# Performance work log

Hardware: AMD Instinct MI355X
Metric: run time of the kernel (lower is better)

The kernel has to match this reference:

```python
import jax, jax.numpy as jnp
import numpy as np

NUM_CONTROL_POINTS = 4
# Standard Catmull-Rom spline basis (rows map [1, t, t^2, t^3] monomials to control points)
CATMULL_ROM_BASIS = 0.5 * np.array(
    [[0.0, 2.0, 0.0, 0.0],
     [-1.0, 0.0, 1.0, 0.0],
     [2.0, -5.0, 4.0, -1.0],
     [-1.0, 3.0, -3.0, 1.0]], dtype=np.float32)

BATCH, IN_F, OUT_F = 1024, 512, 512


def setup_inputs() -> dict:
    key = jax.random.key(0)
    k1, k2, k3, k4 = jax.random.split(key, 4)
    inp = jax.random.normal(k1, (BATCH, IN_F), dtype=jnp.float32)
    # phase spans [0, 2*pi) so both spline segments (mask = phase < 1.5*pi) are exercised
    phase = jax.random.uniform(k2, (BATCH,), dtype=jnp.float32) * (2.0 * jnp.pi)
    bound = 1.0 / np.sqrt(IN_F)
    weights = jax.random.uniform(k3, (NUM_CONTROL_POINTS, OUT_F, IN_F), dtype=jnp.float32,
                                 minval=-bound, maxval=bound)
    biases = jax.random.uniform(k4, (NUM_CONTROL_POINTS, OUT_F), dtype=jnp.float32,
                                minval=-bound, maxval=bound)
    return {"input": inp, "phase": phase, "weights": weights, "biases": biases}


def _spline_coeffs(phase):
    # Faithful to the original (including its overwrite bug): tt = [1, t^2, t^3, 0]
    basis = jnp.asarray(CATMULL_ROM_BASIS, dtype=phase.dtype)
    t0 = phase / (1.5 * jnp.pi)
    t1 = (phase - 0.5 * jnp.pi) / (1.5 * jnp.pi)
    ones, zeros = jnp.ones_like(phase), jnp.zeros_like(phase)
    tt0 = jnp.stack([ones, t0 * t0, t0 ** 3, zeros], axis=1)  # (B,4)
    tt1 = jnp.stack([ones, t1 * t1, t1 ** 3, zeros], axis=1)  # (B,4)
    mask = (phase < 1.5 * jnp.pi)[:, None]
    # Selecting per-sample coefficients before the weight contraction is exactly
    # equivalent to where(mask, tt0@B@W, tt1@B@W) since the map is linear in tt.
    return jnp.where(mask, tt0 @ basis, tt1 @ basis)  # (B,4) control-point coeffs


def reference(input, phase, weights, biases):
    c = _spline_coeffs(phase)                       # (B,4)
    # Fused form: apply the 4 shared control-point linear layers, then blend,
    # avoiding the (B,out,in) per-sample weight tensor. Same math as
    # (tt@B@W).reshape(B,out,in) @ input[:,:,None] + b.
    y4 = jnp.einsum('bi,coi->bco', input, weights)  # (B,4,out)
    out = jnp.einsum('bc,bco->bo', c, y4) + c @ biases  # (B,out)
    return out
```

## Files before the change

### kernel.cpp

```cpp
#include <hip/hip_runtime.h>


#define BATCH 1024
#define IN_F  512
#define OUT_F 512

constexpr int BM = 32;
constexpr int BO = 32;
constexpr int BK = 32;
constexpr int KITERS = IN_F / BK;
constexpr int A_ELEMS = BM * BK;
constexpr int TILE_ELEMS = (BM + 4 * BO) * BK;
constexpr int NVEC = TILE_ELEMS / 8;

typedef unsigned short u16;
typedef u16    u16x8  __attribute__((ext_vector_type(8)));
typedef __bf16 bf16x8 __attribute__((ext_vector_type(8)));
typedef float  f32x4  __attribute__((ext_vector_type(4)));

__device__ __forceinline__ u16 f2bits(float f) {
  union { float f; unsigned int u; } v; v.f = f;
  unsigned int u = v.u;
  unsigned int r = u + 0x7fffu + ((u >> 16) & 1u);
  return (u16)(r >> 16);
}

__global__ __launch_bounds__(256)
void PhaseLinear_kernel(const float* __restrict__ inp, const float* __restrict__ ph,
                        const float* __restrict__ wts, const float* __restrict__ bia,
                        float* __restrict__ outp) {
  __shared__ alignas(16) u16 sT[2][TILE_ELEMS];
  __shared__ float sCoef[BM][4];

  const int tid = threadIdx.x;
  const int wv  = tid >> 6;
  const int wo  = wv & 1;
  const int wm  = wv >> 1;
  const int l   = tid & 63;
  const int o0  = blockIdx.x * BO;
  const int b0  = blockIdx.y * BM;

  if (tid < BM) {
    const float PI = 3.14159265358979323846f;
    float p  = ph[b0 + tid];
    float t  = (p < 1.5f * PI) ? (p / (1.5f * PI)) : ((p - 0.5f * PI) / (1.5f * PI));
    float t2 = t * t, t3 = t2 * t;
    sCoef[tid][0] = t3 - 0.5f * t2;
    sCoef[tid][1] = 1.0f - 2.5f * t3;
    sCoef[tid][2] = 0.5f * t2 + 2.0f * t3;
    sCoef[tid][3] = -0.5f * t3;
  }

  const int nv = (tid < NVEC - 512) ? 3 : 2;
  const float* src[3];
  int loff[3];
#pragma unroll
  for (int j = 0; j < 3; ++j) {
    int v = tid + j * 256;
    if (v >= NVEC) { src[j] = inp; loff[j] = 0; continue; }
    int e = v * 8;
    loff[j] = e;
    if (e < A_ELEMS) {
      int row = e >> 5, col = e & 31;
      src[j] = inp + (size_t)(b0 + row) * IN_F + col;
    } else {
      int ep = e - A_ELEMS;
      int r = ep >> 5, col = ep & 31;
      int c = r >> 5, oo = r & 31;
      src[j] = wts + ((size_t)c * OUT_F + o0 + oo) * IN_F + col;
    }
  }

  f32x4 regs[3][2];
#pragma unroll
  for (int j = 0; j < 3; ++j)
    if (j < nv) {
      regs[j][0] = *(const f32x4*)(src[j]);
      regs[j][1] = *(const f32x4*)(src[j] + 4);
    }

  f32x4 acc[4];
#pragma unroll
  for (int c = 0; c < 4; ++c) acc[c] = (f32x4){0.f, 0.f, 0.f, 0.f};

  const int q = l >> 4;
  const int n = l & 15;

  for (int kk = 0; kk < KITERS; ++kk) {
    const int bsel = kk & 1;
    u16* buf = &sT[bsel][0];
#pragma unroll
    for (int j = 0; j < 3; ++j)
      if (j < nv) {
        u16x8 pk;
#pragma unroll
        for (int x = 0; x < 4; ++x) {
          pk[x]     = f2bits(regs[j][0][x]);
          pk[x + 4] = f2bits(regs[j][1][x]);
        }
        *(u16x8*)(buf + loff[j]) = pk;
      }
    if (kk + 1 < KITERS) {
#pragma unroll
      for (int j = 0; j < 3; ++j)
        if (j < nv) {
          regs[j][0] = *(const f32x4*)(src[j] + (kk + 1) * BK);
          regs[j][1] = *(const f32x4*)(src[j] + (kk + 1) * BK + 4);
        }
    }
    __syncthreads();
    const u16* pA = buf;
    const u16* pW = buf + A_ELEMS;
    bf16x8 a0 = *(const bf16x8*)(pA + (wm * 16 + n) * BK + q * 8);
#pragma unroll
    for (int c = 0; c < 4; ++c) {
      bf16x8 wf = *(const bf16x8*)(pW + (c * 32 + wo * 16 + n) * BK + q * 8);
      acc[c] = __builtin_amdgcn_mfma_f32_16x16x32_bf16(a0, wf, acc[c], 0, 0, 0);
    }
  }

  const int o = o0 + wo * 16 + n;
  float bs[4];
#pragma unroll
  for (int c = 0; c < 4; ++c) bs[c] = bia[c * OUT_F + o];

#pragma unroll
  for (int r = 0; r < 4; ++r) {
    const int bl = wm * 16 + q * 4 + r;
    float v = 0.f;
#pragma unroll
    for (int c = 0; c < 4; ++c)
      v += sCoef[bl][c] * (acc[c][r] + bs[c]);
    outp[(size_t)(b0 + bl) * OUT_F + o] = v;
  }
}

extern "C" void kernel_launch(void* const* d_in, const int* in_sizes, int n_in,
                              void* d_out, int out_size, void* d_ws, size_t ws_size,
                              hipStream_t stream) {
  const float* inp = (const float*)d_in[0];
  const float* ph  = (const float*)d_in[1];
  const float* wts = (const float*)d_in[2];
  const float* bia = (const float*)d_in[3];
  float* outp = (float*)d_out;

  dim3 grid(OUT_F / BO, BATCH / BM);
  PhaseLinear_kernel<<<grid, 256, 0, stream>>>(inp, ph, wts, bia, outp);
}
```

Measured before the change: 72.66 us.

## Split K across warps with smaller output tile and shared-memory reduction

Halves the output tile width to 16 and assigns the two pairs of waves to separate halves of the K dimension, so each block does half as many K iterations. The two partial sums are combined through a shared-memory buffer before the spline blend and the store. This doubles the grid size for more parallelism and shortens the serial K loop. The cost is an extra reduction step and barrier, and each input tile is re-read by twice as many blocks.

```diff
diff --git a/kernel.cpp b/kernel.cpp
--- a/kernel.cpp
+++ b/kernel.cpp
@@ -6,11 +6,13 @@
 #define OUT_F 512
 
 constexpr int BM = 32;
-constexpr int BO = 32;
+constexpr int BO = 16;
 constexpr int BK = 32;
-constexpr int KITERS = IN_F / BK;
-constexpr int A_ELEMS = BM * BK;
-constexpr int TILE_ELEMS = (BM + 4 * BO) * BK;
+constexpr int KW = IN_F / 2;
+constexpr int KITERS = KW / BK;
+constexpr int A_ELEMS = 2 * BM * BK;
+constexpr int W_ELEMS = 2 * 4 * BO * BK;
+constexpr int TILE_ELEMS = A_ELEMS + W_ELEMS;
 constexpr int NVEC = TILE_ELEMS / 8;
 
 typedef unsigned short u16;
@@ -31,11 +33,12 @@
                         float* __restrict__ outp) {
   __shared__ alignas(16) u16 sT[2][TILE_ELEMS];
   __shared__ float sCoef[BM][4];
+  __shared__ float sRed[2][64][16];
 
   const int tid = threadIdx.x;
   const int wv  = tid >> 6;
-  const int wo  = wv & 1;
-  const int wm  = wv >> 1;
+  const int wm  = wv & 1;
+  const int ks  = wv >> 1;
   const int l   = tid & 63;
   const int o0  = blockIdx.x * BO;
   const int b0  = blockIdx.y * BM;
@@ -51,33 +54,32 @@
     sCoef[tid][3] = -0.5f * t3;
   }
 
-  const int nv = (tid < NVEC - 512) ? 3 : 2;
   const float* src[3];
   int loff[3];
 #pragma unroll
   for (int j = 0; j < 3; ++j) {
     int v = tid + j * 256;
-    if (v >= NVEC) { src[j] = inp; loff[j] = 0; continue; }
     int e = v * 8;
     loff[j] = e;
     if (e < A_ELEMS) {
-      int row = e >> 5, col = e & 31;
-      src[j] = inp + (size_t)(b0 + row) * IN_F + col;
+      int w = e >> 10, rem = e & 1023;
+      int row = rem >> 5, k = rem & 31;
+      src[j] = inp + (size_t)(b0 + row) * IN_F + w * KW + k;
     } else {
-      int ep = e - A_ELEMS;
-      int r = ep >> 5, col = ep & 31;
-      int c = r >> 5, oo = r & 31;
-      src[j] = wts + ((size_t)c * OUT_F + o0 + oo) * IN_F + col;
+      int e2 = e - A_ELEMS;
+      int w = e2 >> 11, rem = e2 & 2047;
+      int r = rem >> 5, k = rem & 31;
+      int c = r >> 4, oo = r & 15;
+      src[j] = wts + ((size_t)c * OUT_F + o0 + oo) * IN_F + w * KW + k;
     }
   }
 
   f32x4 regs[3][2];
 #pragma unroll
-  for (int j = 0; j < 3; ++j)
-    if (j < nv) {
-      regs[j][0] = *(const f32x4*)(src[j]);
-      regs[j][1] = *(const f32x4*)(src[j] + 4);
-    }
+  for (int j = 0; j < 3; ++j) {
+    regs[j][0] = *(const f32x4*)(src[j]);
+    regs[j][1] = *(const f32x4*)(src[j] + 4);
+  }
 
   f32x4 acc[4];
 #pragma unroll
@@ -90,48 +92,56 @@
     const int bsel = kk & 1;
     u16* buf = &sT[bsel][0];
 #pragma unroll
-    for (int j = 0; j < 3; ++j)
-      if (j < nv) {
-        u16x8 pk;
+    for (int j = 0; j < 3; ++j) {
+      u16x8 pk;
 #pragma unroll
-        for (int x = 0; x < 4; ++x) {
-          pk[x]     = f2bits(regs[j][0][x]);
-          pk[x + 4] = f2bits(regs[j][1][x]);
-        }
-        *(u16x8*)(buf + loff[j]) = pk;
+      for (int x = 0; x < 4; ++x) {
+        pk[x]     = f2bits(regs[j][0][x]);
+        pk[x + 4] = f2bits(regs[j][1][x]);
       }
+      *(u16x8*)(buf + loff[j]) = pk;
+    }
     if (kk + 1 < KITERS) {
 #pragma unroll
-      for (int j = 0; j < 3; ++j)
-        if (j < nv) {
-          regs[j][0] = *(const f32x4*)(src[j] + (kk + 1) * BK);
-          regs[j][1] = *(const f32x4*)(src[j] + (kk + 1) * BK + 4);
-        }
+      for (int j = 0; j < 3; ++j) {
+        regs[j][0] = *(const f32x4*)(src[j] + (kk + 1) * BK);
+        regs[j][1] = *(const f32x4*)(src[j] + (kk + 1) * BK + 4);
+      }
     }
     __syncthreads();
-    const u16* pA = buf;
-    const u16* pW = buf + A_ELEMS;
-    bf16x8 a0 = *(const bf16x8*)(pA + (wm * 16 + n) * BK + q * 8);
+    bf16x8 a0 = *(const bf16x8*)(buf + ks * 1024 + (wm * 16 + n) * BK + q * 8);
+    const u16* pW = buf + A_ELEMS + ks * 2048;
 #pragma unroll
     for (int c = 0; c < 4; ++c) {
-      bf16x8 wf = *(const bf16x8*)(pW + (c * 32 + wo * 16 + n) * BK + q * 8);
+      bf16x8 wf = *(const bf16x8*)(pW + c * 512 + n * BK + q * 8);
       acc[c] = __builtin_amdgcn_mfma_f32_16x16x32_bf16(a0, wf, acc[c], 0, 0, 0);
     }
   }
 
-  const int o = o0 + wo * 16 + n;
-  float bs[4];
+  if (ks == 1) {
 #pragma unroll
-  for (int c = 0; c < 4; ++c) bs[c] = bia[c * OUT_F + o];
+    for (int c = 0; c < 4; ++c)
+#pragma unroll
+      for (int r = 0; r < 4; ++r) sRed[wm][l][c * 4 + r] = acc[c][r];
+  }
+  __syncthreads();
+  if (ks == 0) {
+    const int o = o0 + n;
+    float bs[4];
+#pragma unroll
+    for (int c = 0; c < 4; ++c) bs[c] = bia[c * OUT_F + o];
 
 #pragma unroll
-  for (int r = 0; r < 4; ++r) {
-    const int bl = wm * 16 + q * 4 + r;
-    float v = 0.f;
+    for (int r = 0; r < 4; ++r) {
+      const int bl = wm * 16 + q * 4 + r;
+      float v = 0.f;
 #pragma unroll
-    for (int c = 0; c < 4; ++c)
-      v += sCoef[bl][c] * (acc[c][r] + bs[c]);
-    outp[(size_t)(b0 + bl) * OUT_F + o] = v;
+      for (int c = 0; c < 4; ++c) {
+        float s = acc[c][r] + sRed[wm][l][c * 4 + r];
+        v += sCoef[bl][c] * (s + bs[c]);
+      }
+      outp[(size_t)(b0 + bl) * OUT_F + o] = v;
+    }
   }
 }
 
```

New measurement: 71.97 us. About the same (-0.9%).
